# Kernel optimization log

Measured on AMD Instinct MI355X. Metric: run time of the kernel, lower is better.

Reference implementation:

```python
import jax, jax.numpy as jnp
import numpy as np
from math import factorial

ZS = np.array([0, 1])
NZ = 2
N_BASIS = 3
N_CHAN = N_BASIS * N_BASIS
N_RBF = 8
MAX_L = 3
CUTOFF = 5.5
P_CUT = 6
N_NODES = 10000
N_EDGES = 100000


def _lxlylz_list(max_l):
    out = []
    for l in range(max_l + 1):
        for lx in range(l, -1, -1):
            for ly in range(l - lx, -1, -1):
                out.append((lx, ly, l - lx - ly))
    return out

LXLYLZ = np.array(_lxlylz_list(MAX_L), dtype=np.int32)  # [n_ang, 3]; (0,0,0) is index 0
N_ANG = LXLYLZ.shape[0]  # 20 for max_l=3

# nu=2 rotational invariants: for each l>0, monomial indices with lx+ly+lz==l and multinomial prefactors
NU2 = []
for l in range(1, MAX_L + 1):
    idx = [i for i in range(N_ANG) if int(LXLYLZ[i].sum()) == l]
    pref = np.array([factorial(l) / (factorial(int(LXLYLZ[i][0])) * factorial(int(LXLYLZ[i][1])) * factorial(int(LXLYLZ[i][2]))) for i in idx], dtype=np.float32)
    NU2.append((np.array(idx, dtype=np.int32), pref))


def setup_inputs() -> dict:
    key = jax.random.key(0)
    ks = jax.random.split(key, 6)
    positions = jax.random.normal(ks[0], (N_NODES, 3), jnp.float32)
    atomic_numbers = jax.random.randint(ks[1], (N_NODES,), 0, NZ)
    edge_index = jax.random.randint(ks[2], (2, N_EDGES), 0, N_NODES)
    edge_lengths = jax.random.uniform(ks[3], (N_EDGES,), jnp.float32, 0.5, CUTOFF)
    edge_vectors = jax.random.normal(ks[4], (N_EDGES, 3), jnp.float32)
    W_embed = jax.random.normal(ks[5], (NZ, N_BASIS), jnp.float32) / np.sqrt(NZ)
    return dict(positions=positions, atomic_numbers=atomic_numbers, edge_index=edge_index,
                edge_lengths=edge_lengths, edge_vectors=edge_vectors, W_embed=W_embed)


def reference(positions, atomic_numbers, edge_index, edge_lengths, edge_vectors, W_embed):
    n_nodes = positions.shape[0]
    # node one-hot over zs -> linear embedding
    one_hot = (atomic_numbers[:, None] == jnp.asarray(ZS)[None, :]).astype(W_embed.dtype)
    emb = one_hot @ W_embed  # [N, n_basis]
    # directed edge-type encoding: outer product of sender/receiver embeddings
    enc = (emb[edge_index[0]][:, :, None] * emb[edge_index[1]][:, None, :]).reshape(-1, N_CHAN)  # [E, c]
    # Bessel radial basis * polynomial cutoff
    r = edge_lengths
    n = jnp.arange(1, N_RBF + 1, dtype=r.dtype)
    radial = jnp.sqrt(2.0 / CUTOFF) * jnp.sin(n[None, :] * jnp.pi * r[:, None] / CUTOFF) / r[:, None]
    u = r / CUTOFF
    p = P_CUT
    fc = (1.0 - 0.5 * (p + 1) * (p + 2) * u ** p + p * (p + 2) * u ** (p + 1)
          - 0.5 * p * (p + 1) * u ** (p + 2)) * (u < 1.0)
    radial = radial * fc[:, None]  # [E, n_rbf]
    # angular monomials x^lx y^ly z^lz of unit edge vectors
    unit = edge_vectors / jnp.linalg.norm(edge_vectors, axis=-1, keepdims=True)
    ang = jnp.prod(unit[:, None, :] ** jnp.asarray(LXLYLZ)[None, :, :], axis=-1)  # [E, n_ang]
    # fused 3-tensor edge product then scatter-sum to receiver nodes
    edge_attr = jnp.einsum('er,ea,ec->erac', radial, ang, enc)  # [E, n_rbf, n_ang, c]
    A = jax.ops.segment_sum(edge_attr, edge_index[1], num_segments=n_nodes)  # node_feat_A
    # symmetrize to invariants: nu=1 (l=0 monomial) + nu=2 per-l invariants
    feats = [A[:, :, 0:1, :]]
    for idx, pref in NU2:
        sel = A[:, :, jnp.asarray(idx), :]
        feats.append(jnp.sum(jnp.asarray(pref)[None, None, :, None] * sel * sel, axis=2, keepdims=True))
    B = jnp.concatenate(feats, axis=2)  # node_feat_B: [N, n_rbf, 1+max_l, c]
    return B
```

## Files before the change

kernel.cpp:

```cpp
#include <hip/hip_runtime.h>


#define NN    10000
#define NE    100000
#define NRBF  8
#define NANG  20
#define NCHAN 9
#define CAP   64
#define BROW  28
#define NODES_PER_BLK 4
#define INV_CUT  (1.0f/5.5f)
#define PI_F     3.14159265358979323846f
#define RAD_NORM 0.6030226891555273f

#define WSYNC() asm volatile("s_waitcnt lgkmcnt(0)" ::: "memory")

__launch_bounds__(256, 4)
__global__ void scatter_k(const int* __restrict__ an, const int* __restrict__ ei,
                          int* __restrict__ cnt, int* __restrict__ lst) {
    int e = blockIdx.x * blockDim.x + threadIdx.x;
    if (e >= NE) return;
    int src = ei[e];
    int dst = ei[NE + e];
    int zs  = an[src];
    int pos = atomicAdd(&cnt[dst], 1);
    if (pos < CAP) lst[dst * CAP + pos] = e | (zs << 20);
}

__launch_bounds__(256, 5)
__global__ void node_k(const int* __restrict__ an, const float* __restrict__ elen,
                       const float* __restrict__ evec, const float* __restrict__ W,
                       const int* __restrict__ cnt, const int* __restrict__ lst,
                       float* __restrict__ out)
{
    __shared__ float sB[NODES_PER_BLK * CAP * BROW];

    const int tid  = threadIdx.x;
    const int w    = tid >> 6;
    const int lane = tid & 63;
    const int n    = blockIdx.x * NODES_PER_BLK + w;

    float* Bw = &sB[w * CAP * BROW];
    float* sA = Bw;

    const int vv  = lst[n * CAP + lane];
    const int dgr = cnt[n];
    const int zd  = an[n];
    const float W0=W[0], W1=W[1], W2=W[2], W3=W[3], W4=W[4], W5=W[5];

    const int deg = (dgr > CAP) ? CAP : dgr;

    int zsv = 0;
    if (lane < deg) {
        const int eid = vv & 0xFFFFF;
        zsv = vv >> 20;

        const float r  = elen[eid];
        const float vx = evec[3*eid+0], vy = evec[3*eid+1], vz = evec[3*eid+2];
        const float inv = rsqrtf(vx*vx + vy*vy + vz*vz);
        const float x = vx*inv, y = vy*inv, z = vz*inv;

        const float u  = r * INV_CUT;
        const float u2 = u*u, u6 = u2*u2*u2;
        const float fc = (u < 1.0f) ? (1.0f - 28.0f*u6 + 48.0f*u6*u - 21.0f*u6*u2)
                                    : 0.0f;
        const float scale = RAD_NORM * fc / r;
        float s1, c1;
        sincosf(PI_F * u, &s1, &c1);
        const float twoc = 2.0f * c1;
        float sp = 0.0f, s = s1;
        float rad[8];
        #pragma unroll
        for (int k = 0; k < 8; ++k) {
            rad[k] = scale * s;
            const float sn = twoc * s - sp;
            sp = s; s = sn;
        }

        const float xx = x*x, xy = x*y, xz = x*z, yy = y*y, yz = y*z, zz = z*z;
        float* B = &Bw[lane * BROW];
        *(float4*)&B[0]  = make_float4(rad[0], rad[1], rad[2], rad[3]);
        *(float4*)&B[4]  = make_float4(rad[4], rad[5], rad[6], rad[7]);
        *(float4*)&B[8]  = make_float4(1.0f, x, y, z);
        *(float4*)&B[12] = make_float4(xx, xy, xz, yy);
        *(float4*)&B[16] = make_float4(yz, zz, x*xx, y*xx);
        *(float4*)&B[20] = make_float4(z*xx, x*yy, x*yz, x*zz);
        *(float4*)&B[24] = make_float4(y*yy, z*yy, y*zz, z*zz);
    }
    const unsigned long long zmask = __ballot(zsv != 0);
    WSYNC();

    const int r0 = lane & 7;
    const int a0 = lane >> 3;
    float s00=0.f, s01=0.f, s02=0.f;
    float s10=0.f, s11=0.f, s12=0.f;

    int e = 0;
    for (; e + 1 < deg; e += 2) {
        const float* Ba = &Bw[e * BROW];
        const float* Bb = &Bw[(e+1) * BROW];
        const float z1a = (float)((zmask >> e) & 1ULL);
        const float z1b = (float)((zmask >> (e+1)) & 1ULL);
        const float z0a = 1.0f - z1a, z0b = 1.0f - z1b;
        const float rda = Ba[r0],      rdb = Bb[r0];
        const float v0a = rda * Ba[8 + a0],  v0b = rdb * Bb[8 + a0];
        const float v1a = rda * Ba[16 + a0], v1b = rdb * Bb[16 + a0];
        s00 = fmaf(v0a, z0a, s00); s10 = fmaf(v0a, z1a, s10);
        s01 = fmaf(v1a, z0a, s01); s11 = fmaf(v1a, z1a, s11);
        s00 = fmaf(v0b, z0b, s00); s10 = fmaf(v0b, z1b, s10);
        s01 = fmaf(v1b, z0b, s01); s11 = fmaf(v1b, z1b, s11);
        if (lane < 32) {
            const float v2a = rda * Ba[24 + a0], v2b = rdb * Bb[24 + a0];
            s02 = fmaf(v2a, z0a, s02); s12 = fmaf(v2a, z1a, s12);
            s02 = fmaf(v2b, z0b, s02); s12 = fmaf(v2b, z1b, s12);
        }
    }
    if (e < deg) {
        const float* B = &Bw[e * BROW];
        const float z1 = (float)((zmask >> e) & 1ULL);
        const float z0 = 1.0f - z1;
        const float rd = B[r0];
        const float v0 = rd * B[8 + a0];
        const float v1 = rd * B[16 + a0];
        s00 = fmaf(v0, z0, s00); s10 = fmaf(v0, z1, s10);
        s01 = fmaf(v1, z0, s01); s11 = fmaf(v1, z1, s11);
        if (lane < 32) {
            const float v2 = rd * B[24 + a0];
            s02 = fmaf(v2, z0, s02); s12 = fmaf(v2, z1, s12);
        }
    }
    WSYNC();

    const float wd0 = zd ? W3 : W0, wd1 = zd ? W4 : W1, wd2 = zd ? W5 : W2;
    {
        const float t00 = W0*s00 + W3*s10, t01 = W1*s00 + W4*s10, t02 = W2*s00 + W5*s10;
        float* Ap = &sA[r0*180 + a0*9];
        Ap[0]=t00*wd0; Ap[1]=t00*wd1; Ap[2]=t00*wd2;
        Ap[3]=t01*wd0; Ap[4]=t01*wd1; Ap[5]=t01*wd2;
        Ap[6]=t02*wd0; Ap[7]=t02*wd1; Ap[8]=t02*wd2;
    }
    {
        const float t10 = W0*s01 + W3*s11, t11 = W1*s01 + W4*s11, t12 = W2*s01 + W5*s11;
        float* Ap = &sA[r0*180 + (8 + a0)*9];
        Ap[0]=t10*wd0; Ap[1]=t10*wd1; Ap[2]=t10*wd2;
        Ap[3]=t11*wd0; Ap[4]=t11*wd1; Ap[5]=t11*wd2;
        Ap[6]=t12*wd0; Ap[7]=t12*wd1; Ap[8]=t12*wd2;
    }
    if (lane < 32) {
        const float t20 = W0*s02 + W3*s12, t21 = W1*s02 + W4*s12, t22 = W2*s02 + W5*s12;
        float* Ap = &sA[r0*180 + (16 + a0)*9];
        Ap[0]=t20*wd0; Ap[1]=t20*wd1; Ap[2]=t20*wd2;
        Ap[3]=t21*wd0; Ap[4]=t21*wd1; Ap[5]=t21*wd2;
        Ap[6]=t22*wd0; Ap[7]=t22*wd1; Ap[8]=t22*wd2;
    }
    WSYNC();

    for (int o = lane; o < NRBF*4*NCHAN; o += 64) {
        const int r = o / 36, rem = o - r*36, l = rem / 9, c = rem - (rem/9)*9;
        const float* Ar = &sA[r * 180 + c];
        float val;
        if (l == 0) {
            val = Ar[0];
        } else if (l == 1) {
            const float v1 = Ar[9], v2 = Ar[18], v3 = Ar[27];
            val = v1*v1 + v2*v2 + v3*v3;
        } else if (l == 2) {
            const float v0=Ar[36], v1=Ar[45], v2=Ar[54],
                        v3=Ar[63], v4=Ar[72], v5=Ar[81];
            val = v0*v0 + 2.0f*(v1*v1 + v2*v2 + v4*v4) + v3*v3 + v5*v5;
        } else {
            const float w0=Ar[90],  w1=Ar[99],  w2=Ar[108], w3=Ar[117], w4=Ar[126];
            const float w5=Ar[135], w6=Ar[144], w7=Ar[153], w8=Ar[162], w9=Ar[171];
            val = w0*w0 + w6*w6 + w9*w9
                + 3.0f*(w1*w1 + w2*w2 + w3*w3 + w5*w5 + w7*w7 + w8*w8)
                + 6.0f*w4*w4;
        }
        out[n * (NRBF*4*NCHAN) + o] = val;
    }
}

extern "C" void kernel_launch(void* const* d_in, const int* in_sizes, int n_in,
                              void* d_out, int out_size, void* d_ws, size_t ws_size,
                              hipStream_t stream) {
    const int*   an   = (const int*)d_in[1];
    const int*   ei   = (const int*)d_in[2];
    const float* elen = (const float*)d_in[3];
    const float* evec = (const float*)d_in[4];
    const float* W    = (const float*)d_in[5];
    float* out = (float*)d_out;

    int* cnt = (int*)d_ws;
    int* lst = cnt + NN;

    hipMemsetAsync(cnt, 0, NN * sizeof(int), stream);
    scatter_k<<<(NE + 255)/256, 256, 0, stream>>>(an, ei, cnt, lst);
    node_k<<<NN / NODES_PER_BLK, 256, 0, stream>>>(an, elen, evec, W, cnt, lst, out);
}
```

Before: 90.77 us.

## Compute invariants in registers with wave shuffles instead of LDS staging

Replaces the LDS write of the full A tensor and the strided per-output gather with a register-level computation. Each lane squares its own angular projections, applies the multinomial prefactor from packed constants and buckets the result by l. Lanes with the same radial index then reduce through xor shuffles, and the factorized receiver weight is applied as squared scalars. This removes two LDS round trips and the divide-heavy output indexing, but concentrates the output writes in 8 lanes doing float4 stores.

```diff
diff --git a/kernel.cpp b/kernel.cpp
--- a/kernel.cpp
+++ b/kernel.cpp
@@ -41,12 +41,11 @@
     const int n    = blockIdx.x * NODES_PER_BLK + w;
 
     float* Bw = &sB[w * CAP * BROW];
-    float* sA = Bw;
 
     const int vv  = lst[n * CAP + lane];
     const int dgr = cnt[n];
     const int zd  = an[n];
-    const float W0=W[0], W1=W[1], W2=W[2], W3=W[3], W4=W[4], W5=W[5];
+    const float Wa0=W[0], Wa1=W[1], Wa2=W[2], Wa3=W[3], Wa4=W[4], Wa5=W[5];
 
     const int deg = (dgr > CAP) ? CAP : dgr;
 
@@ -129,53 +128,53 @@
             s02 = fmaf(v2, z0, s02); s12 = fmaf(v2, z1, s12);
         }
     }
-    WSYNC();
 
-    const float wd0 = zd ? W3 : W0, wd1 = zd ? W4 : W1, wd2 = zd ? W5 : W2;
-    {
-        const float t00 = W0*s00 + W3*s10, t01 = W1*s00 + W4*s10, t02 = W2*s00 + W5*s10;
-        float* Ap = &sA[r0*180 + a0*9];
-        Ap[0]=t00*wd0; Ap[1]=t00*wd1; Ap[2]=t00*wd2;
-        Ap[3]=t01*wd0; Ap[4]=t01*wd1; Ap[5]=t01*wd2;
-        Ap[6]=t02*wd0; Ap[7]=t02*wd1; Ap[8]=t02*wd2;
+    const float pf0 = (float)((0x12211110u >> (4*a0)) & 0xF);
+    const float pf1 = (float)((0x36333112u >> (4*a0)) & 0xF);
+    const float pf2 = (float)((0x1331u     >> (4*a0)) & 0xF);
+
+    const float WL[3] = {Wa0, Wa1, Wa2};
+    const float WH[3] = {Wa3, Wa4, Wa5};
+    float T0k[3], b1[3], b2[3], b3[3];
+    #pragma unroll
+    for (int i = 0; i < 3; ++i) {
+        const float T0 = WL[i]*s00 + WH[i]*s10;
+        const float T1 = WL[i]*s01 + WH[i]*s11;
+        const float T2 = WL[i]*s02 + WH[i]*s12;
+        T0k[i] = T0;
+        const float q0 = pf0 * T0 * T0;
+        const float q1 = pf1 * T1 * T1;
+        const float q2 = pf2 * T2 * T2;
+        b1[i] = (a0 >= 1 && a0 <= 3) ? q0 : 0.f;
+        b2[i] = ((a0 >= 4) ? q0 : 0.f) + ((a0 <= 1) ? q1 : 0.f);
+        b3[i] = ((a0 >= 2) ? q1 : 0.f) + q2;
     }
-    {
-        const float t10 = W0*s01 + W3*s11, t11 = W1*s01 + W4*s11, t12 = W2*s01 + W5*s11;
-        float* Ap = &sA[r0*180 + (8 + a0)*9];
-        Ap[0]=t10*wd0; Ap[1]=t10*wd1; Ap[2]=t10*wd2;
-        Ap[3]=t11*wd0; Ap[4]=t11*wd1; Ap[5]=t11*wd2;
-        Ap[6]=t12*wd0; Ap[7]=t12*wd1; Ap[8]=t12*wd2;
+
+    #pragma unroll
+    for (int m = 8; m <= 32; m <<= 1) {
+        #pragma unroll
+        for (int i = 0; i < 3; ++i) {
+            b1[i] += __shfl_xor(b1[i], m, 64);
+            b2[i] += __shfl_xor(b2[i], m, 64);
+            b3[i] += __shfl_xor(b3[i], m, 64);
+        }
     }
-    if (lane < 32) {
-        const float t20 = W0*s02 + W3*s12, t21 = W1*s02 + W4*s12, t22 = W2*s02 + W5*s12;
-        float* Ap = &sA[r0*180 + (16 + a0)*9];
-        Ap[0]=t20*wd0; Ap[1]=t20*wd1; Ap[2]=t20*wd2;
-        Ap[3]=t21*wd0; Ap[4]=t21*wd1; Ap[5]=t21*wd2;
-        Ap[6]=t22*wd0; Ap[7]=t22*wd1; Ap[8]=t22*wd2;
-    }
-    WSYNC();
 
-    for (int o = lane; o < NRBF*4*NCHAN; o += 64) {
-        const int r = o / 36, rem = o - r*36, l = rem / 9, c = rem - (rem/9)*9;
-        const float* Ar = &sA[r * 180 + c];
-        float val;
-        if (l == 0) {
-            val = Ar[0];
-        } else if (l == 1) {
-            const float v1 = Ar[9], v2 = Ar[18], v3 = Ar[27];
-            val = v1*v1 + v2*v2 + v3*v3;
-        } else if (l == 2) {
-            const float v0=Ar[36], v1=Ar[45], v2=Ar[54],
-                        v3=Ar[63], v4=Ar[72], v5=Ar[81];
-            val = v0*v0 + 2.0f*(v1*v1 + v2*v2 + v4*v4) + v3*v3 + v5*v5;
-        } else {
-            const float w0=Ar[90],  w1=Ar[99],  w2=Ar[108], w3=Ar[117], w4=Ar[126];
-            const float w5=Ar[135], w6=Ar[144], w7=Ar[153], w8=Ar[162], w9=Ar[171];
-            val = w0*w0 + w6*w6 + w9*w9
-                + 3.0f*(w1*w1 + w2*w2 + w3*w3 + w5*w5 + w7*w7 + w8*w8)
-                + 6.0f*w4*w4;
+    if (lane < 8) {
+        const float wd0 = zd ? Wa3 : Wa0, wd1 = zd ? Wa4 : Wa1, wd2 = zd ? Wa5 : Wa2;
+        const float e0 = wd0*wd0, e1 = wd1*wd1, e2 = wd2*wd2;
+        float v[36];
+        #pragma unroll
+        for (int i = 0; i < 3; ++i) {
+            v[     i*3+0] = T0k[i]*wd0; v[     i*3+1] = T0k[i]*wd1; v[     i*3+2] = T0k[i]*wd2;
+            v[ 9 + i*3+0] = b1[i]*e0;   v[ 9 + i*3+1] = b1[i]*e1;   v[ 9 + i*3+2] = b1[i]*e2;
+            v[18 + i*3+0] = b2[i]*e0;   v[18 + i*3+1] = b2[i]*e1;   v[18 + i*3+2] = b2[i]*e2;
+            v[27 + i*3+0] = b3[i]*e0;   v[27 + i*3+1] = b3[i]*e1;   v[27 + i*3+2] = b3[i]*e2;
         }
-        out[n * (NRBF*4*NCHAN) + o] = val;
+        float4* O = (float4*)(out + (long)n * (NRBF*4*NCHAN) + lane * 36);
+        #pragma unroll
+        for (int k = 0; k < 9; ++k)
+            O[k] = make_float4(v[4*k], v[4*k+1], v[4*k+2], v[4*k+3]);
     }
 }
 
```

Measured after the change: 87.84 us. -3.2%, faster.
